# Optimization experiments

Hardware: AMD Instinct MI355X
Metric: run time of the kernel (lower is better)

Reference implementation:

```python
import jax, jax.numpy as jnp
import jax.scipy as jsp
import numpy as np

LAMBDA_1 = 0.1
LAMBDA_2 = 0.005
EPS_DIAG = 1e-6      # jitter added to covariance diagonal
LOG_2PI_CONST = 2 * 3.14159  # torch code uses 3.14159, not math.pi

B, K, D = 262144, 8, 32


def setup_inputs() -> dict:
    key = jax.random.key(0)
    k1, k2, k3 = jax.random.split(key, 3)
    gamma = jax.random.uniform(k1, (B, K), dtype=jnp.float32)
    features = jax.random.normal(k2, (B, D), dtype=jnp.float32)
    reconstruction_error = jax.random.uniform(k3, (B,), dtype=jnp.float32)
    return {"gamma": gamma, "features": features,
            "reconstruction_error": reconstruction_error}


def _gmm_parameters(gamma, features):
    # gamma: [B,K], features: [B,D]
    gsum = jnp.sum(gamma, axis=0)                              # [K]
    phi = jnp.mean(gamma, axis=0)                              # [K]
    mu = jnp.einsum('bk,bd->kd', gamma, features) / (gsum[:, None] + 1e-8)  # [K,D]
    diff = features[:, None, :] - mu[None, :, :]               # [B,K,D]
    sigma = jnp.einsum('bk,bkd,bke->kde', gamma, diff, diff)   # [K,D,D]
    sigma = sigma / (gsum[:, None, None] + 1e-8)
    sigma = sigma + EPS_DIAG * jnp.eye(sigma.shape[-1], dtype=sigma.dtype)[None]
    return phi, mu, sigma, diff


def _energy(diff, phi, sigma):
    # Batched Cholesky over K tiny SPD matrices (sigma is PD by construction).
    feature_dim = sigma.shape[-1]
    L = jnp.linalg.cholesky(sigma)                             # [K,D,D]
    eye = jnp.eye(feature_dim, dtype=sigma.dtype)
    Linv = jax.vmap(lambda l: jsp.linalg.solve_triangular(l, eye, lower=True))(L)
    inv_sigma = jnp.einsum('kij,kil->kjl', Linv, Linv)         # (L L^T)^-1
    log_det = 2.0 * jnp.sum(jnp.log(jnp.diagonal(L, axis1=-2, axis2=-1)), axis=-1)  # [K]
    mahal = jnp.einsum('bkd,kde,bke->bk', diff, inv_sigma, diff)  # [B,K]
    log_2pi = feature_dim * jnp.log(jnp.asarray(LOG_2PI_CONST, dtype=diff.dtype))
    log_prob = -0.5 * (mahal + log_det[None, :] + log_2pi)     # [B,K]
    wlp = jnp.log(phi + 1e-10)[None, :] + log_prob             # [B,K]
    m = jnp.max(wlp, axis=1)                                   # [B]
    sum_exp = jnp.sum(jnp.exp(wlp - m[:, None]), axis=1)
    total_energy = -(m + jnp.log(sum_exp + 1e-10))
    return jnp.where(jnp.isfinite(total_energy), total_energy,
                     jnp.zeros_like(total_energy))


def reference(gamma, features, reconstruction_error):
    phi, mu, sigma, diff = _gmm_parameters(gamma, features)
    reconstruction_loss = jnp.mean(reconstruction_error)
    energy_loss = jnp.mean(_energy(diff, phi, sigma))
    diag = jnp.diagonal(sigma, axis1=-2, axis2=-1)
    singularity_loss = jnp.sum(1.0 / (diag + 1e-8))
    return reconstruction_loss + LAMBDA_1 * energy_loss + LAMBDA_2 * singularity_loss
```

## Files before the change

kernel.cpp:

```cpp
#include <hip/hip_runtime.h>

using v8h  = __attribute__((ext_vector_type(8))) __fp16;
using h2   = __attribute__((ext_vector_type(2))) __fp16;
using v16f = __attribute__((ext_vector_type(16))) float;
using v4f  = __attribute__((ext_vector_type(4))) float;

#define B_SIZE 262144
#define WS_S2    0
#define WS_S1    8192
#define WS_GS    8448
#define WS_SING  8456
#define WS_C1    8464
#define WS_L16   8736
#define WS_ENP   13184
#define WS_RCP   14208
#define WS_PART  15360
#define PART_STRIDE 8464
#define MOM_BLK  256
#define EN_BLK   1024

union PkU { h2 p[4]; v8h v; };

__device__ __forceinline__ float lane_bcast(float v, int l) {
  return __builtin_bit_cast(float,
      __builtin_amdgcn_readlane(__builtin_bit_cast(int, v), l));
}

__global__ __launch_bounds__(512, 4) void k_moments(
    const float* __restrict__ gamma, const float* __restrict__ feat,
    float* __restrict__ part) {
  __shared__ float s2l[8 * 32 * 33];
  __shared__ float s1l[8 * 32];
  __shared__ float gsl[8];
  const int tid = threadIdx.x, lane = tid & 63, w = tid >> 6;
  const int c = lane & 31, half = lane >> 5;
  const int ROWS = B_SIZE / MOM_BLK;
  const int base = blockIdx.x * ROWS;

  v16f acc;
#pragma unroll
  for (int r = 0; r < 16; ++r) acc[r] = 0.f;
  float s1a = 0.f, ga = 0.f;

  for (int ch = 0; ch < ROWS / 16; ++ch) {
    const int rb = base + ch * 16 + half * 8;
    float fc[8], g8[8];
#pragma unroll
    for (int j = 0; j < 8; ++j) {
      fc[j] = feat[(size_t)(rb + j) * 32 + c];
      g8[j] = gamma[(size_t)(rb + j) * 8 + w];
    }
    PkU fp, gp;
#pragma unroll
    for (int jj = 0; jj < 4; ++jj) {
      fp.p[jj] = __builtin_amdgcn_cvt_pkrtz(fc[2 * jj], fc[2 * jj + 1]);
      gp.p[jj] = __builtin_amdgcn_cvt_pkrtz(g8[2 * jj], g8[2 * jj + 1]);
    }
#pragma unroll
    for (int j = 0; j < 8; ++j) {
      s1a = fmaf(g8[j], fc[j], s1a);
      ga += g8[j];
    }
    const v8h af = gp.v * fp.v;
    acc = __builtin_amdgcn_mfma_f32_32x32x16_f16(af, fp.v, acc, 0, 0, 0);
  }

#pragma unroll
  for (int r = 0; r < 16; ++r) {
    const int row = (r & 3) + 8 * (r >> 2) + 4 * half;
    s2l[w * 1056 + row * 33 + c] = acc[r];
  }
  s1a += __shfl_xor(s1a, 32);
  ga  += __shfl_xor(ga, 32);
  if (half == 0) s1l[w * 32 + c] = s1a;
  if (lane == 0) gsl[w] = ga;
  __syncthreads();

  float* pb = part + (size_t)blockIdx.x * PART_STRIDE;
  for (int t = tid; t < 8192; t += 512) {
    const int k = t >> 10, row = (t >> 5) & 31, cc = t & 31;
    pb[t] = s2l[k * 1056 + row * 33 + cc];
  }
  if (tid < 256) pb[8192 + tid] = s1l[tid];
  if (tid < 8) pb[8448 + tid] = gsl[tid];
}

__global__ void k_reduce(const float* __restrict__ part, float* __restrict__ ws) {
  const int t = blockIdx.x * 256 + threadIdx.x;
  if (t >= 8456) return;
  float s = 0.f;
  for (int b = 0; b < MOM_BLK; ++b) s += part[(size_t)b * PART_STRIDE + t];
  ws[t] = s;
}

__global__ __launch_bounds__(64, 1) void k_prepare(float* __restrict__ ws) {
  __shared__ float T[32 * 33];
  const int k = blockIdx.x;
  const int i = threadIdx.x & 63;
  const int ri = i & 31;
  const bool act = i < 32;

  const float gs = ws[WS_GS + k];
  const float denom = gs + 1e-8f;
  const float rden = __builtin_amdgcn_rcpf(denom);
  const float s1i = ws[WS_S1 + k * 32 + ri];
  const float mu_i = s1i * rden;

  float a[32];
  {
    const float4* s2p = (const float4*)(ws + WS_S2 + k * 1024 + ri * 32);
    float4 q4[8];
#pragma unroll
    for (int t = 0; t < 8; ++t) q4[t] = s2p[t];
#pragma unroll
    for (int t = 0; t < 8; ++t) {
      a[4 * t + 0] = q4[t].x; a[4 * t + 1] = q4[t].y;
      a[4 * t + 2] = q4[t].z; a[4 * t + 3] = q4[t].w;
    }
  }
  float sing = 0.f;
#pragma unroll
  for (int j = 0; j < 32; ++j) {
    const float muj = lane_bcast(mu_i, j);
    const float s1j = lane_bcast(s1i, j);
    float sig = a[j] - mu_i * s1j - muj * s1i + gs * mu_i * muj;
    sig = sig * rden + ((ri == j) ? 1e-6f : 0.f);
    a[j] = sig;
    if (ri == j) sing = __builtin_amdgcn_rcpf(sig + 1e-8f);
  }
  if (!act) sing = 0.f;
#pragma unroll
  for (int m = 1; m < 64; m <<= 1) sing += __shfl_xor(sing, m);
  if (i == 0) ws[WS_SING + k] = sing;

  float logdet = 0.f;
#pragma unroll
  for (int j = 0; j < 32; ++j) {
    const float ajj = lane_bcast(a[j], j);
    const float ljj = __builtin_amdgcn_sqrtf(ajj);
    const float rljj = __builtin_amdgcn_rcpf(ljj);
    logdet += __logf(ajj);
    const float lij = (ri == j) ? ljj : ((ri > j) ? a[j] * rljj : 0.f);
    a[j] = lij;
#pragma unroll
    for (int p = j + 1; p < 32; ++p) {
      const float lpj = lane_bcast(lij, p);
      a[p] = fmaf(-lij, lpj, a[p]);
    }
  }

  const int c = ri;
  float x[32];
#pragma unroll
  for (int r = 0; r < 32; ++r) {
    float s = (r == c) ? 1.f : 0.f;
#pragma unroll
    for (int p = 0; p < r; ++p) {
      const float lrp = lane_bcast(a[p], r);
      s = fmaf(-lrp, x[p], s);
    }
    x[r] = s * __builtin_amdgcn_rcpf(lane_bcast(a[r], r));
  }

  if (act) {
#pragma unroll
    for (int r = 0; r < 32; ++r) T[r * 33 + c] = x[r];
  }
  __syncthreads();
  float xr[32];
#pragma unroll
  for (int p = 0; p < 32; ++p) xr[p] = T[ri * 33 + p];

  __fp16* l16 = (__fp16*)(ws + WS_L16);
  if (act) {
#pragma unroll
    for (int t = 0; t < 4; ++t) {
      PkU h4;
#pragma unroll
      for (int u = 0; u < 4; ++u)
        h4.p[u] = __builtin_amdgcn_cvt_pkrtz(xr[8 * t + 2 * u], xr[8 * t + 2 * u + 1]);
      *(v8h*)(l16 + (size_t)(k * 32 + ri) * 32 + 8 * t) = h4.v;
    }
  }

  float lm = 0.f;
#pragma unroll
  for (int p = 0; p < 32; ++p) lm = fmaf(xr[p], lane_bcast(mu_i, p), lm);

  float lm2 = act ? lm * lm : 0.f;
#pragma unroll
  for (int m = 1; m < 64; m <<= 1) lm2 += __shfl_xor(lm2, m);

  float q = 0.f;
#pragma unroll
  for (int j = 0; j < 32; ++j) q = fmaf(x[j], lane_bcast(lm, j), q);
  if (act) {
    l16[(size_t)(256 + k) * 32 + c] = (__fp16)q;
    l16[(size_t)(264 + k) * 32 + c] = (__fp16)0.f;
  }

  if (i == 0) {
    const float phi = gs * (1.f / (float)B_SIZE);
    ws[WS_C1 + k] =
        __logf(phi + 1e-10f) - 0.5f * (logdet + 32.f * logf(6.28318f)) - 0.5f * lm2;
  }
}

__global__ __launch_bounds__(256, 4) void k_energy(
    const float* __restrict__ feat, const float* __restrict__ rec,
    const float* __restrict__ ws, float* __restrict__ aws) {
  __shared__ float ben[4], brc[4];
  const int tid = threadIdx.x, lane = tid & 63, wv = tid >> 6;
  const int gw = blockIdx.x * 4 + wv;
  const int ROWS = B_SIZE / (EN_BLK * 4);
  const int base = gw * ROWS;
  const int cl = lane & 15, g = lane >> 4;
  const int p0 = g * 8;

  const __fp16* l16 = (const __fp16*)(ws + WS_L16);
  v8h mf[17];
#pragma unroll
  for (int t = 0; t < 17; ++t)
    mf[t] = *(const v8h*)(l16 + (size_t)(16 * t + cl) * 32 + p0);
  float c1[8];
#pragma unroll
  for (int k = 0; k < 8; ++k) c1[k] = ws[WS_C1 + k];

  float en_acc = 0.f, rv_acc = 0.f;
  const v4f zf = {0.f, 0.f, 0.f, 0.f};

  for (int ch = 0; ch < ROWS / 16; ++ch) {
    const int b0 = base + ch * 16;
    const size_t row = (size_t)(b0 + cl) * 32;
    const float4 fa = *(const float4*)(feat + row + p0);
    const float4 fb = *(const float4*)(feat + row + p0 + 4);
    PkU af;
    af.p[0] = __builtin_amdgcn_cvt_pkrtz(fa.x, fa.y);
    af.p[1] = __builtin_amdgcn_cvt_pkrtz(fa.z, fa.w);
    af.p[2] = __builtin_amdgcn_cvt_pkrtz(fb.x, fb.y);
    af.p[3] = __builtin_amdgcn_cvt_pkrtz(fb.z, fb.w);

    float zk[8];
#pragma unroll
    for (int k = 0; k < 8; ++k) zk[k] = 0.f;
    float yq[4];

#pragma unroll
    for (int t = 0; t < 17; ++t) {
      const v4f y = __builtin_amdgcn_mfma_f32_16x16x32_f16(mf[t], af.v, zf, 0, 0, 0);
      if (t < 16) {
#pragma unroll
        for (int r = 0; r < 4; ++r) zk[t >> 1] = fmaf(y[r], y[r], zk[t >> 1]);
      } else {
#pragma unroll
        for (int r = 0; r < 4; ++r) yq[r] = y[r];
      }
    }
#pragma unroll
    for (int m = 16; m < 64; m <<= 1)
#pragma unroll
      for (int k = 0; k < 8; ++k) zk[k] += __shfl_xor(zk[k], m);

    float mx = -3.0e38f, s = 0.f;
#pragma unroll
    for (int k = 0; k < 8; ++k) {
      const float yp = __shfl(yq[k & 3], cl + ((k >> 2) << 4));
      const float w = c1[k] + yp - 0.5f * zk[k];
      const float mn = fmaxf(mx, w);
      s = s * __expf(mx - mn) + __expf(w - mn);
      mx = mn;
    }
    float en = -(mx + __logf(s + 1e-10f));
    en = (en == en && en < 1e38f && en > -1e38f) ? en : 0.f;
    if (lane < 16) {
      en_acc += en;
      rv_acc += rec[b0 + cl];
    }
  }
#pragma unroll
  for (int m = 32; m; m >>= 1) {
    en_acc += __shfl_down(en_acc, m);
    rv_acc += __shfl_down(rv_acc, m);
  }
  if (lane == 0) { ben[wv] = en_acc; brc[wv] = rv_acc; }
  __syncthreads();
  if (tid == 0) {
    aws[WS_ENP + blockIdx.x] = ben[0] + ben[1] + ben[2] + ben[3];
    aws[WS_RCP + blockIdx.x] = brc[0] + brc[1] + brc[2] + brc[3];
  }
}

__global__ void k_final(const float* __restrict__ ws, float* __restrict__ out) {
  __shared__ float r1[256], r2[256];
  const int tid = threadIdx.x;
  float e = 0.f, r = 0.f;
  for (int i = tid; i < EN_BLK; i += 256) {
    e += ws[WS_ENP + i];
    r += ws[WS_RCP + i];
  }
  r1[tid] = e; r2[tid] = r;
  __syncthreads();
  for (int s = 128; s > 0; s >>= 1) {
    if (tid < s) { r1[tid] += r1[tid + s]; r2[tid] += r2[tid + s]; }
    __syncthreads();
  }
  if (tid == 0) {
    float sing = 0.f;
    for (int t = 0; t < 8; ++t) sing += ws[WS_SING + t];
    const float recm = r2[0] * (1.f / (float)B_SIZE);
    const float enm  = r1[0] * (1.f / (float)B_SIZE);
    out[0] = recm + 0.1f * enm + 0.005f * sing;
  }
}

extern "C" void kernel_launch(void* const* d_in, const int* in_sizes, int n_in,
                              void* d_out, int out_size, void* d_ws, size_t ws_size,
                              hipStream_t stream) {
  const float* gamma = (const float*)d_in[0];
  const float* feat  = (const float*)d_in[1];
  const float* rec   = (const float*)d_in[2];
  float* ws = (float*)d_ws;
  float* out = (float*)d_out;

  hipLaunchKernelGGL(k_moments, dim3(MOM_BLK), dim3(512), 0, stream,
                     gamma, feat, ws + WS_PART);
  hipLaunchKernelGGL(k_reduce, dim3(34), dim3(256), 0, stream, ws + WS_PART, ws);
  hipLaunchKernelGGL(k_prepare, dim3(8), dim3(64), 0, stream, ws);
  hipLaunchKernelGGL(k_energy, dim3(EN_BLK), dim3(256), 0, stream, feat, rec, ws, ws);
  hipLaunchKernelGGL(k_final, dim3(1), dim3(256), 0, stream, ws, out);
}
```

Baseline: 153.0 us.

## Double moment-kernel waves per block and split partial reduction into two stages

The moments kernel now runs 1024 threads per block. Two groups of 8 waves each process half of the block's 1024 rows and are summed in LDS before the partials are written. The single serial 256-way partial reduction becomes a 34x8-block first pass over 32 partials each, then a second 8-way pass. This is meant to raise parallelism in the moment accumulation and cut the long serial loop in the reduce kernel, at the cost of one extra kernel launch, a workspace buffer and doubled LDS use per block.

```diff
diff --git a/kernel.cpp b/kernel.cpp
--- a/kernel.cpp
+++ b/kernel.cpp
@@ -15,6 +15,7 @@
 #define WS_ENP   13184
 #define WS_RCP   14208
 #define WS_PART  15360
+#define WS_PART2 2182144
 #define PART_STRIDE 8464
 #define MOM_BLK  256
 #define EN_BLK   1024
@@ -26,29 +27,30 @@
       __builtin_amdgcn_readlane(__builtin_bit_cast(int, v), l));
 }
 
-__global__ __launch_bounds__(512, 4) void k_moments(
+__global__ __launch_bounds__(1024, 4) void k_moments(
     const float* __restrict__ gamma, const float* __restrict__ feat,
     float* __restrict__ part) {
-  __shared__ float s2l[8 * 32 * 33];
-  __shared__ float s1l[8 * 32];
-  __shared__ float gsl[8];
+  __shared__ float s2l[16 * 1056];
+  __shared__ float s1l[16 * 32];
+  __shared__ float gsl[16];
   const int tid = threadIdx.x, lane = tid & 63, w = tid >> 6;
+  const int k = w & 7, hsel = w >> 3;
   const int c = lane & 31, half = lane >> 5;
-  const int ROWS = B_SIZE / MOM_BLK;
-  const int base = blockIdx.x * ROWS;
+  const int base = blockIdx.x * 1024 + hsel * 512;
 
   v16f acc;
 #pragma unroll
   for (int r = 0; r < 16; ++r) acc[r] = 0.f;
   float s1a = 0.f, ga = 0.f;
 
-  for (int ch = 0; ch < ROWS / 16; ++ch) {
+#pragma unroll 2
+  for (int ch = 0; ch < 32; ++ch) {
     const int rb = base + ch * 16 + half * 8;
     float fc[8], g8[8];
 #pragma unroll
     for (int j = 0; j < 8; ++j) {
       fc[j] = feat[(size_t)(rb + j) * 32 + c];
-      g8[j] = gamma[(size_t)(rb + j) * 8 + w];
+      g8[j] = gamma[(size_t)(rb + j) * 8 + k];
     }
     PkU fp, gp;
 #pragma unroll
@@ -77,19 +79,31 @@
   __syncthreads();
 
   float* pb = part + (size_t)blockIdx.x * PART_STRIDE;
-  for (int t = tid; t < 8192; t += 512) {
-    const int k = t >> 10, row = (t >> 5) & 31, cc = t & 31;
-    pb[t] = s2l[k * 1056 + row * 33 + cc];
-  }
-  if (tid < 256) pb[8192 + tid] = s1l[tid];
-  if (tid < 8) pb[8448 + tid] = gsl[tid];
-}
-
-__global__ void k_reduce(const float* __restrict__ part, float* __restrict__ ws) {
+  for (int t = tid; t < 8192; t += 1024) {
+    const int kk = t >> 10, row = (t >> 5) & 31, cc = t & 31;
+    pb[t] = s2l[kk * 1056 + row * 33 + cc] + s2l[(kk + 8) * 1056 + row * 33 + cc];
+  }
+  if (tid < 256) pb[8192 + tid] = s1l[tid] + s1l[tid + 256];
+  if (tid < 8) pb[8448 + tid] = gsl[tid] + gsl[tid + 8];
+}
+
+__global__ void k_reduce(const float* __restrict__ part, float* __restrict__ p2) {
+  const int t = blockIdx.x * 256 + threadIdx.x;
+  if (t >= 8456) return;
+  const int y = blockIdx.y;
+  float s = 0.f;
+#pragma unroll 8
+  for (int b = y * 32; b < y * 32 + 32; ++b)
+    s += part[(size_t)b * PART_STRIDE + t];
+  p2[(size_t)y * PART_STRIDE + t] = s;
+}
+
+__global__ void k_reduce2(const float* __restrict__ p2, float* __restrict__ ws) {
   const int t = blockIdx.x * 256 + threadIdx.x;
   if (t >= 8456) return;
   float s = 0.f;
-  for (int b = 0; b < MOM_BLK; ++b) s += part[(size_t)b * PART_STRIDE + t];
+#pragma unroll
+  for (int y = 0; y < 8; ++y) s += p2[(size_t)y * PART_STRIDE + t];
   ws[t] = s;
 }
 
@@ -322,9 +336,11 @@
   float* ws = (float*)d_ws;
   float* out = (float*)d_out;
 
-  hipLaunchKernelGGL(k_moments, dim3(MOM_BLK), dim3(512), 0, stream,
+  hipLaunchKernelGGL(k_moments, dim3(MOM_BLK), dim3(1024), 0, stream,
                      gamma, feat, ws + WS_PART);
-  hipLaunchKernelGGL(k_reduce, dim3(34), dim3(256), 0, stream, ws + WS_PART, ws);
+  hipLaunchKernelGGL(k_reduce, dim3(34, 8), dim3(256), 0, stream,
+                     ws + WS_PART, ws + WS_PART2);
+  hipLaunchKernelGGL(k_reduce2, dim3(34), dim3(256), 0, stream, ws + WS_PART2, ws);
   hipLaunchKernelGGL(k_prepare, dim3(8), dim3(64), 0, stream, ws);
   hipLaunchKernelGGL(k_energy, dim3(EN_BLK), dim3(256), 0, stream, feat, rec, ws, ws);
   hipLaunchKernelGGL(k_final, dim3(1), dim3(256), 0, stream, ws, out);
```

Measured after the change: 132.4 us. 1.16x faster.
